# Kernel tuning notes

Hardware: AMD Instinct MI355X
Metric: run time of the kernel (lower is better)

## Reference

```python
import jax, jax.numpy as jnp
import numpy as np

K = 32  # attention rank
EPS = 1e-6

def setup_inputs() -> dict:
    key = jax.random.key(0)
    k1, k2 = jax.random.split(key)
    N, d = 500000, 256
    x = jax.random.normal(k1, (N, d), dtype=jnp.float32)
    # Xavier-normal-ish scale for Linear(d, 4k)
    W = jax.random.normal(k2, (d, 4 * K), dtype=jnp.float32) * jnp.sqrt(2.0 / (d + 4 * K))
    b = jnp.zeros((4 * K,), dtype=jnp.float32)
    return {"x": x, "W": W, "b": b}

def reference(x, W, b):
    # X = ReLU(x @ W + b): [N, 4k]
    X = jax.nn.relu(x @ W + b)
    U = X[:, :K]            # [N, k]
    V = X[:, K:2 * K]       # [N, k]
    Z = X[:, 2 * K:3 * K]   # [N, k]
    T = X[:, 3 * K:]        # [N, k]
    # joint_normalize2: norm_factor = sum(U @ (V^T @ ones)) / N + eps
    s = V.sum(axis=0)                              # [k] == V^T @ ones
    norm_factor = (U @ s).sum() / U.shape[0] + EPS  # scalar
    D = 1.0 / norm_factor
    # low-rank attention: U @ (V^T @ Z), inner [k, k] GEMM kept tiny
    VtZ = jnp.einsum('nk,nj->kj', V, Z)  # [k, k]
    res = U @ VtZ                        # [N, k]
    return jnp.concatenate((res * D, T), axis=1)  # [N, 2k]
```

## Files before the change

### kernel.cpp

```cpp
#include <hip/hip_runtime.h>
#include <hip/hip_bf16.h>

#define DK 256
#define NC 128
#define EPSV 1e-6f

typedef __bf16 bf16x8 __attribute__((ext_vector_type(8)));
typedef __bf16 bf16x4 __attribute__((ext_vector_type(4)));
typedef float f32x4 __attribute__((ext_vector_type(4)));


__global__ __launch_bounds__(512, 4) void k_gemm(
    const float* __restrict__ x, const float* __restrict__ W,
    const float* __restrict__ bias, float* __restrict__ out,
    float* __restrict__ accg, int N)
{
  __shared__ __bf16 Wlds[32768];
  __shared__ __bf16 Vt[32 * 72];
  __shared__ __bf16 Zt[32 * 72];
  __shared__ float  redS[64];

  const int tid  = threadIdx.x;
  const int wave = tid >> 6;
  const int lane = tid & 63;
  const int quad = lane >> 4;
  const int l16  = lane & 15;
  const int mw   = wave >> 1;
  const int nw   = wave & 1;

  for (int f = tid; f < 4096; f += 512) {
    const int n  = f & 127;
    const int qk = f >> 7;
    const int k0 = (qk >> 2) * 32 + (qk & 3) * 8;
    bf16x8 w;
    #pragma unroll
    for (int j = 0; j < 8; ++j) w[j] = (__bf16)W[(size_t)(k0 + j) * NC + n];
    *(bf16x8*)&Wlds[f * 8] = w;
  }
  float bias4[4];
  #pragma unroll
  for (int ntl = 0; ntl < 4; ++ntl) bias4[ntl] = bias[nw * 64 + ntl * 16 + l16];
  __syncthreads();

  float usumv[2] = {0.f, 0.f};
  float ssumv[2] = {0.f, 0.f};
  f32x4 vacc = (f32x4){0.f, 0.f, 0.f, 0.f};
  const int mt = wave >> 1, nt = wave & 1;

  const int nchunks = (N + 63) >> 6;
  for (int c = blockIdx.x; c < nchunks; c += gridDim.x) {
    const int rbase = c << 6;
    const int arow  = rbase + mw * 16 + l16;
    const bool rv   = arow < N;
    const float* xr = x + (size_t)arow * DK;

    f32x4 xv[16];
    #pragma unroll
    for (int kk = 0; kk < 8; ++kk) {
      const int koff = kk * 32 + quad * 8;
      xv[2 * kk]     = rv ? *(const f32x4*)(xr + koff)     : (f32x4){0.f,0.f,0.f,0.f};
      xv[2 * kk + 1] = rv ? *(const f32x4*)(xr + koff + 4) : (f32x4){0.f,0.f,0.f,0.f};
    }

    f32x4 acc[4];
    #pragma unroll
    for (int t = 0; t < 4; ++t) acc[t] = (f32x4){0.f, 0.f, 0.f, 0.f};

    #pragma unroll
    for (int kk = 0; kk < 8; ++kk) {
      bf16x8 af;
      af[0] = (__bf16)xv[2*kk].x;   af[1] = (__bf16)xv[2*kk].y;
      af[2] = (__bf16)xv[2*kk].z;   af[3] = (__bf16)xv[2*kk].w;
      af[4] = (__bf16)xv[2*kk+1].x; af[5] = (__bf16)xv[2*kk+1].y;
      af[6] = (__bf16)xv[2*kk+1].z; af[7] = (__bf16)xv[2*kk+1].w;
      #pragma unroll
      for (int ntl = 0; ntl < 4; ++ntl) {
        const bf16x8 bf = *(const bf16x8*)&Wlds[(((kk << 2) | quad) * 128
                                                + nw * 64 + ntl * 16 + l16) * 8];
        acc[ntl] = __builtin_amdgcn_mfma_f32_16x16x32_bf16(af, bf, acc[ntl], 0, 0, 0);
      }
    }

    #pragma unroll
    for (int ntl = 0; ntl < 4; ++ntl) {
      float v4[4];
      #pragma unroll
      for (int r = 0; r < 4; ++r) {
        const int grow = rbase + mw * 16 + quad * 4 + r;
        float v = acc[ntl][r] + bias4[ntl];
        v = fmaxf(v, 0.f);
        if (grow >= N) v = 0.f;
        v4[r] = v;
      }
      const int grow0 = rbase + mw * 16 + quad * 4;
      if (nw == 0) {
        if (ntl < 2) {
          #pragma unroll
          for (int r = 0; r < 4; ++r) {
            if (grow0 + r < N) out[(size_t)(grow0 + r) * 64 + ntl * 16 + l16] = v4[r];
            usumv[ntl] += v4[r];
          }
        } else {
          ssumv[ntl - 2] += v4[0] + v4[1] + v4[2] + v4[3];
          bf16x4 pv;
          pv[0] = (__bf16)v4[0]; pv[1] = (__bf16)v4[1];
          pv[2] = (__bf16)v4[2]; pv[3] = (__bf16)v4[3];
          const int col = (ntl - 2) * 16 + l16;
          const int lrow = mw * 16 + quad * 4;
          *(bf16x4*)&Vt[col * 72 + lrow] = pv;
        }
      } else {
        if (ntl < 2) {
          bf16x4 pv;
          pv[0] = (__bf16)v4[0]; pv[1] = (__bf16)v4[1];
          pv[2] = (__bf16)v4[2]; pv[3] = (__bf16)v4[3];
          const int col = ntl * 16 + l16;
          const int lrow = mw * 16 + quad * 4;
          *(bf16x4*)&Zt[col * 72 + lrow] = pv;
        } else {
          #pragma unroll
          for (int r = 0; r < 4; ++r)
            if (grow0 + r < N) out[(size_t)(grow0 + r) * 64 + 32 + (ntl - 2) * 16 + l16] = v4[r];
        }
      }
    }
    __syncthreads();
    if (wave < 4) {
      #pragma unroll
      for (int ks = 0; ks < 2; ++ks) {
        const bf16x8 av = *(const bf16x8*)&Vt[(mt * 16 + l16) * 72 + ks * 32 + quad * 8];
        const bf16x8 bz = *(const bf16x8*)&Zt[(nt * 16 + l16) * 72 + ks * 32 + quad * 8];
        vacc = __builtin_amdgcn_mfma_f32_16x16x32_bf16(av, bz, vacc, 0, 0, 0);
      }
    }
    __syncthreads();
  }

  if (tid < 64) redS[tid] = 0.f;
  __syncthreads();
  if (nw == 0) {
    atomicAdd(&redS[l16],      usumv[0]);
    atomicAdd(&redS[16 + l16], usumv[1]);
    atomicAdd(&redS[32 + l16], ssumv[0]);
    atomicAdd(&redS[48 + l16], ssumv[1]);
  }
  __syncthreads();
  if (tid < 64) atomicAdd(&accg[tid], redS[tid]);
  if (wave < 4) {
    #pragma unroll
    for (int r = 0; r < 4; ++r)
      atomicAdd(&accg[64 + (mt * 16 + quad * 4 + r) * 32 + nt * 16 + l16], vacc[r]);
  }
}

__global__ void k_norm(float* __restrict__ accg, int N) {
  const int t = threadIdx.x;
  float p = 0.f;
  if (t < 32) p = accg[t] * accg[32 + t];
  #pragma unroll
  for (int off = 16; off >= 1; off >>= 1) p += __shfl_down(p, off);
  if (t == 0) accg[1088] = 1.0f / (p / (float)N + EPSV);
}

__global__ __launch_bounds__(256) void k_res(float* __restrict__ out,
                                             const float* __restrict__ accg, int N) {
  __shared__ float Ms[32 * 33];
  __shared__ float Us[64 * 33];
  const float D = accg[1088];
  for (int i = threadIdx.x; i < 1024; i += 256)
    Ms[(i >> 5) * 33 + (i & 31)] = accg[64 + i] * D;
  const int j  = threadIdx.x & 31;
  const int r0 = threadIdx.x >> 5;
  const int rbase = blockIdx.x * 64;
  #pragma unroll
  for (int i = 0; i < 8; ++i) {
    const int lr = r0 + i * 8;
    const int row = rbase + lr;
    Us[lr * 33 + j] = (row < N) ? out[(size_t)row * 64 + j] : 0.f;
  }
  __syncthreads();
  #pragma unroll
  for (int i = 0; i < 8; ++i) {
    const int lr = r0 + i * 8;
    const int row = rbase + lr;
    if (row < N) {
      float a = 0.f;
      #pragma unroll
      for (int k = 0; k < 32; ++k) a += Us[lr * 33 + k] * Ms[k * 33 + j];
      out[(size_t)row * 64 + j] = a;
    }
  }
}

extern "C" void kernel_launch(void* const* d_in, const int* in_sizes, int n_in,
                              void* d_out, int out_size, void* d_ws, size_t ws_size,
                              hipStream_t stream) {
  const float* x    = (const float*)d_in[0];
  const float* W    = (const float*)d_in[1];
  const float* b    = (const float*)d_in[2];
  float* out  = (float*)d_out;
  float* accg = (float*)d_ws;
  const int N = in_sizes[0] / DK;
  const int ngroups = (N + 63) >> 6;

  hipMemsetAsync(accg, 0, 1089 * sizeof(float), stream);
  hipLaunchKernelGGL(k_gemm, dim3(512),     dim3(512), 0, stream, x, W, b, out, accg, N);
  hipLaunchKernelGGL(k_norm, dim3(1),       dim3(64),  0, stream, accg, N);
  hipLaunchKernelGGL(k_res,  dim3(ngroups), dim3(256), 0, stream, out, accg, N);
}
```

Baseline: 786.2 us.

## Give each wave full output columns and accumulate VtZ in registers without barriers

Each wave now computes all 128 projection columns for its own 16 rows, and a chunk grows to 128 rows. This removes the LDS transposes of V and Z and the two block barriers per chunk. The V^T·Z partial product is formed directly from registers with zero-padded MFMA operands, which wastes half the K-dimension of each MFMA. Per-wave partials are reduced across waves once at the end through LDS, reusing the weight buffer. Register pressure per thread grows because the converted A fragments are held across both column halves.

```diff
diff --git a/kernel.cpp b/kernel.cpp
--- a/kernel.cpp
+++ b/kernel.cpp
@@ -16,8 +16,6 @@
     float* __restrict__ accg, int N)
 {
   __shared__ __bf16 Wlds[32768];
-  __shared__ __bf16 Vt[32 * 72];
-  __shared__ __bf16 Zt[32 * 72];
   __shared__ float  redS[64];
 
   const int tid  = threadIdx.x;
@@ -25,8 +23,6 @@
   const int lane = tid & 63;
   const int quad = lane >> 4;
   const int l16  = lane & 15;
-  const int mw   = wave >> 1;
-  const int nw   = wave & 1;
 
   for (int f = tid; f < 4096; f += 512) {
     const int n  = f & 127;
@@ -37,20 +33,22 @@
     for (int j = 0; j < 8; ++j) w[j] = (__bf16)W[(size_t)(k0 + j) * NC + n];
     *(bf16x8*)&Wlds[f * 8] = w;
   }
-  float bias4[4];
-  #pragma unroll
-  for (int ntl = 0; ntl < 4; ++ntl) bias4[ntl] = bias[nw * 64 + ntl * 16 + l16];
+  float bias8[8];
+  #pragma unroll
+  for (int t = 0; t < 8; ++t) bias8[t] = bias[t * 16 + l16];
+  if (tid < 64) redS[tid] = 0.f;
   __syncthreads();
 
   float usumv[2] = {0.f, 0.f};
   float ssumv[2] = {0.f, 0.f};
-  f32x4 vacc = (f32x4){0.f, 0.f, 0.f, 0.f};
-  const int mt = wave >> 1, nt = wave & 1;
-
-  const int nchunks = (N + 63) >> 6;
+  f32x4 vz[4];
+  #pragma unroll
+  for (int t = 0; t < 4; ++t) vz[t] = (f32x4){0.f, 0.f, 0.f, 0.f};
+
+  const int nchunks = (N + 127) >> 7;
   for (int c = blockIdx.x; c < nchunks; c += gridDim.x) {
-    const int rbase = c << 6;
-    const int arow  = rbase + mw * 16 + l16;
+    const int rbase = c << 7;
+    const int arow  = rbase + wave * 16 + l16;
     const bool rv   = arow < N;
     const float* xr = x + (size_t)arow * DK;
 
@@ -61,95 +59,129 @@
       xv[2 * kk]     = rv ? *(const f32x4*)(xr + koff)     : (f32x4){0.f,0.f,0.f,0.f};
       xv[2 * kk + 1] = rv ? *(const f32x4*)(xr + koff + 4) : (f32x4){0.f,0.f,0.f,0.f};
     }
-
-    f32x4 acc[4];
-    #pragma unroll
-    for (int t = 0; t < 4; ++t) acc[t] = (f32x4){0.f, 0.f, 0.f, 0.f};
-
+    bf16x8 af[8];
     #pragma unroll
     for (int kk = 0; kk < 8; ++kk) {
-      bf16x8 af;
-      af[0] = (__bf16)xv[2*kk].x;   af[1] = (__bf16)xv[2*kk].y;
-      af[2] = (__bf16)xv[2*kk].z;   af[3] = (__bf16)xv[2*kk].w;
-      af[4] = (__bf16)xv[2*kk+1].x; af[5] = (__bf16)xv[2*kk+1].y;
-      af[6] = (__bf16)xv[2*kk+1].z; af[7] = (__bf16)xv[2*kk+1].w;
+      bf16x8 a;
+      a[0] = (__bf16)xv[2*kk].x;   a[1] = (__bf16)xv[2*kk].y;
+      a[2] = (__bf16)xv[2*kk].z;   a[3] = (__bf16)xv[2*kk].w;
+      a[4] = (__bf16)xv[2*kk+1].x; a[5] = (__bf16)xv[2*kk+1].y;
+      a[6] = (__bf16)xv[2*kk+1].z; a[7] = (__bf16)xv[2*kk+1].w;
+      af[kk] = a;
+    }
+
+    const int orow0 = rbase + wave * 16 + quad * 4;
+    bf16x4 pv[2], pz[2];
+
+    {
+      f32x4 acc[4];
+      #pragma unroll
+      for (int t = 0; t < 4; ++t) acc[t] = (f32x4){0.f, 0.f, 0.f, 0.f};
+      #pragma unroll
+      for (int kk = 0; kk < 8; ++kk)
+        #pragma unroll
+        for (int ntl = 0; ntl < 4; ++ntl) {
+          const bf16x8 bf = *(const bf16x8*)&Wlds[(((kk << 2) | quad) * 128
+                                                  + ntl * 16 + l16) * 8];
+          acc[ntl] = __builtin_amdgcn_mfma_f32_16x16x32_bf16(af[kk], bf, acc[ntl], 0, 0, 0);
+        }
       #pragma unroll
       for (int ntl = 0; ntl < 4; ++ntl) {
-        const bf16x8 bf = *(const bf16x8*)&Wlds[(((kk << 2) | quad) * 128
-                                                + nw * 64 + ntl * 16 + l16) * 8];
-        acc[ntl] = __builtin_amdgcn_mfma_f32_16x16x32_bf16(af, bf, acc[ntl], 0, 0, 0);
-      }
-    }
-
-    #pragma unroll
-    for (int ntl = 0; ntl < 4; ++ntl) {
-      float v4[4];
-      #pragma unroll
-      for (int r = 0; r < 4; ++r) {
-        const int grow = rbase + mw * 16 + quad * 4 + r;
-        float v = acc[ntl][r] + bias4[ntl];
-        v = fmaxf(v, 0.f);
-        if (grow >= N) v = 0.f;
-        v4[r] = v;
-      }
-      const int grow0 = rbase + mw * 16 + quad * 4;
-      if (nw == 0) {
+        float v4[4];
+        #pragma unroll
+        for (int r = 0; r < 4; ++r) {
+          float v = acc[ntl][r] + bias8[ntl];
+          v = fmaxf(v, 0.f);
+          if (orow0 + r >= N) v = 0.f;
+          v4[r] = v;
+        }
         if (ntl < 2) {
           #pragma unroll
           for (int r = 0; r < 4; ++r) {
-            if (grow0 + r < N) out[(size_t)(grow0 + r) * 64 + ntl * 16 + l16] = v4[r];
+            if (orow0 + r < N) out[(size_t)(orow0 + r) * 64 + ntl * 16 + l16] = v4[r];
             usumv[ntl] += v4[r];
           }
         } else {
           ssumv[ntl - 2] += v4[0] + v4[1] + v4[2] + v4[3];
-          bf16x4 pv;
-          pv[0] = (__bf16)v4[0]; pv[1] = (__bf16)v4[1];
-          pv[2] = (__bf16)v4[2]; pv[3] = (__bf16)v4[3];
-          const int col = (ntl - 2) * 16 + l16;
-          const int lrow = mw * 16 + quad * 4;
-          *(bf16x4*)&Vt[col * 72 + lrow] = pv;
-        }
-      } else {
+          bf16x4 p;
+          p[0] = (__bf16)v4[0]; p[1] = (__bf16)v4[1];
+          p[2] = (__bf16)v4[2]; p[3] = (__bf16)v4[3];
+          pv[ntl - 2] = p;
+        }
+      }
+    }
+    {
+      f32x4 acc[4];
+      #pragma unroll
+      for (int t = 0; t < 4; ++t) acc[t] = (f32x4){0.f, 0.f, 0.f, 0.f};
+      #pragma unroll
+      for (int kk = 0; kk < 8; ++kk)
+        #pragma unroll
+        for (int ntl = 0; ntl < 4; ++ntl) {
+          const bf16x8 bf = *(const bf16x8*)&Wlds[(((kk << 2) | quad) * 128
+                                                  + (ntl + 4) * 16 + l16) * 8];
+          acc[ntl] = __builtin_amdgcn_mfma_f32_16x16x32_bf16(af[kk], bf, acc[ntl], 0, 0, 0);
+        }
+      #pragma unroll
+      for (int ntl = 0; ntl < 4; ++ntl) {
+        float v4[4];
+        #pragma unroll
+        for (int r = 0; r < 4; ++r) {
+          float v = acc[ntl][r] + bias8[ntl + 4];
+          v = fmaxf(v, 0.f);
+          if (orow0 + r >= N) v = 0.f;
+          v4[r] = v;
+        }
         if (ntl < 2) {
-          bf16x4 pv;
-          pv[0] = (__bf16)v4[0]; pv[1] = (__bf16)v4[1];
-          pv[2] = (__bf16)v4[2]; pv[3] = (__bf16)v4[3];
-          const int col = ntl * 16 + l16;
-          const int lrow = mw * 16 + quad * 4;
-          *(bf16x4*)&Zt[col * 72 + lrow] = pv;
+          bf16x4 p;
+          p[0] = (__bf16)v4[0]; p[1] = (__bf16)v4[1];
+          p[2] = (__bf16)v4[2]; p[3] = (__bf16)v4[3];
+          pz[ntl] = p;
         } else {
           #pragma unroll
           for (int r = 0; r < 4; ++r)
-            if (grow0 + r < N) out[(size_t)(grow0 + r) * 64 + 32 + (ntl - 2) * 16 + l16] = v4[r];
+            if (orow0 + r < N)
+              out[(size_t)(orow0 + r) * 64 + 32 + (ntl - 2) * 16 + l16] = v4[r];
         }
       }
     }
-    __syncthreads();
-    if (wave < 4) {
-      #pragma unroll
-      for (int ks = 0; ks < 2; ++ks) {
-        const bf16x8 av = *(const bf16x8*)&Vt[(mt * 16 + l16) * 72 + ks * 32 + quad * 8];
-        const bf16x8 bz = *(const bf16x8*)&Zt[(nt * 16 + l16) * 72 + ks * 32 + quad * 8];
-        vacc = __builtin_amdgcn_mfma_f32_16x16x32_bf16(av, bz, vacc, 0, 0, 0);
+    #pragma unroll
+    for (int vt = 0; vt < 2; ++vt) {
+      bf16x8 av;
+      av[0] = pv[vt][0]; av[1] = pv[vt][1]; av[2] = pv[vt][2]; av[3] = pv[vt][3];
+      av[4] = (__bf16)0.f; av[5] = (__bf16)0.f; av[6] = (__bf16)0.f; av[7] = (__bf16)0.f;
+      #pragma unroll
+      for (int zt = 0; zt < 2; ++zt) {
+        bf16x8 bz;
+        bz[0] = pz[zt][0]; bz[1] = pz[zt][1]; bz[2] = pz[zt][2]; bz[3] = pz[zt][3];
+        bz[4] = (__bf16)0.f; bz[5] = (__bf16)0.f; bz[6] = (__bf16)0.f; bz[7] = (__bf16)0.f;
+        vz[vt * 2 + zt] = __builtin_amdgcn_mfma_f32_16x16x32_bf16(av, bz, vz[vt * 2 + zt], 0, 0, 0);
       }
     }
-    __syncthreads();
-  }
-
-  if (tid < 64) redS[tid] = 0.f;
-  __syncthreads();
-  if (nw == 0) {
-    atomicAdd(&redS[l16],      usumv[0]);
-    atomicAdd(&redS[16 + l16], usumv[1]);
-    atomicAdd(&redS[32 + l16], ssumv[0]);
-    atomicAdd(&redS[48 + l16], ssumv[1]);
+  }
+
+  #pragma unroll
+  for (int t = 0; t < 2; ++t) {
+    atomicAdd(&redS[t * 16 + l16],      usumv[t]);
+    atomicAdd(&redS[32 + t * 16 + l16], ssumv[t]);
   }
   __syncthreads();
   if (tid < 64) atomicAdd(&accg[tid], redS[tid]);
-  if (wave < 4) {
-    #pragma unroll
-    for (int r = 0; r < 4; ++r)
-      atomicAdd(&accg[64 + (mt * 16 + quad * 4 + r) * 32 + nt * 16 + l16], vacc[r]);
+
+  float* vred = (float*)Wlds;
+  #pragma unroll
+  for (int vt = 0; vt < 2; ++vt)
+    #pragma unroll
+    for (int zt = 0; zt < 2; ++zt)
+      #pragma unroll
+      for (int r = 0; r < 4; ++r)
+        vred[wave * 1024 + (vt * 16 + quad * 4 + r) * 32 + zt * 16 + l16] = vz[vt * 2 + zt][r];
+  __syncthreads();
+  for (int e = tid; e < 1024; e += 512) {
+    float s = 0.f;
+    #pragma unroll
+    for (int w = 0; w < 8; ++w) s += vred[w * 1024 + e];
+    atomicAdd(&accg[64 + e], s);
   }
 }
 
```

New measurement: 1.168 ms. 48.6% more time.
